# Optimization experiments

Measured on AMD Instinct MI355X. Metric: run time of the kernel, lower is better.

The kernel has to match this reference:

```python
import jax, jax.numpy as jnp
import numpy as np


def _cdist_p2(x, y):
    # x: [N, t1, h], y: [N, t2, h] -> [N, t1, t2] Euclidean distances
    x2 = jnp.sum(x * x, axis=-1)  # [N, t1]
    y2 = jnp.sum(y * y, axis=-1)  # [N, t2]
    xy = jnp.einsum('nik,njk->nij', x, y)  # [N, t1, t2]
    d2 = x2[:, :, None] + y2[None if False else slice(None), None, :] - 2.0 * xy
    d2 = jnp.maximum(d2, 0.0)
    return jnp.sqrt(d2)


def _solve_relaxed_wmd(scores, axis):
    # argmin + one-hot scatter + (mask*scores).mean() == sum of per-slice minima / scores.size
    idx = jnp.argmin(scores, axis=axis, keepdims=True)
    mins = jnp.take_along_axis(scores, idx, axis=axis)
    return jnp.sum(mins) / scores.size


def setup_inputs() -> dict:
    key = jax.random.key(0)
    kx, ky = jax.random.split(key)
    L, B, t1, t2, h = 4, 16, 1024, 1024, 128
    x = jax.random.normal(kx, (L, B, t1, h), dtype=jnp.float32)
    y = jax.random.normal(ky, (L, B, t2, h), dtype=jnp.float32)
    return {"x": x, "y": y}


def reference(x, y):
    L, B, t1, h = x.shape
    t2 = y.shape[2]
    xf = x.reshape(L * B, t1, h).astype(jnp.float32)
    yf = y.reshape(L * B, t2, h).astype(jnp.float32)
    scores = _cdist_p2(xf, yf)  # [L*B, t1, t2]
    forward_scores = _solve_relaxed_wmd(scores, axis=1)
    backward_scores = _solve_relaxed_wmd(scores, axis=2)
    return jnp.maximum(forward_scores, backward_scores)
```

## Files before the change

### kernel.cpp

```cpp
#include <hip/hip_runtime.h>

#define NB 64
#define T 1024
#define HD 128

#define EINF 0xFF800000u

typedef __attribute__((ext_vector_type(8))) short bf16x8;
typedef __attribute__((ext_vector_type(4))) float f32x4;

static __device__ __forceinline__ short f2bf(float f) {
    unsigned u = __float_as_uint(f);
    u += 0x7FFFu + ((u >> 16) & 1u);
    return (short)(u >> 16);
}
static __device__ __forceinline__ unsigned fenc(float f) {
    unsigned b = __float_as_uint(f);
    return b ^ (unsigned)(((int)b >> 31) | (int)0x80000000);
}
static __device__ __forceinline__ float fdec(unsigned u) {
    unsigned m = (~(unsigned)((int)u >> 31)) | 0x80000000u;
    return __uint_as_float(u ^ m);
}

__global__ void wmd_prep(const float* __restrict__ y, short* __restrict__ ybf,
                         float* __restrict__ y2,
                         unsigned* __restrict__ g_colmin, unsigned* __restrict__ g_rowmin,
                         float* __restrict__ sums, unsigned* __restrict__ batch_cnt,
                         unsigned* __restrict__ g_cnt) {
    int gi = blockIdx.x * 256 + threadIdx.x;
    float4 vy = reinterpret_cast<const float4*>(y)[gi];
    short4 sy;
    sy.x = f2bf(vy.x); sy.y = f2bf(vy.y); sy.z = f2bf(vy.z); sy.w = f2bf(vy.w);
    reinterpret_cast<short4*>(ybf)[gi] = sy;
    float py = vy.x * vy.x + vy.y * vy.y + vy.z * vy.z + vy.w * vy.w;
    py += __shfl_xor(py, 1);  py += __shfl_xor(py, 2);  py += __shfl_xor(py, 4);
    py += __shfl_xor(py, 8);  py += __shfl_xor(py, 16);
    if ((threadIdx.x & 31) == 0) y2[gi >> 5] = py;
    if (gi < NB * T) { g_colmin[gi] = EINF; g_rowmin[gi] = EINF; }
    if (gi < 2) sums[gi] = 0.f;
    if (gi >= 4 && gi < 4 + NB) batch_cnt[gi - 4] = 0u;
    if (gi == 4 + NB) g_cnt[0] = 0u;
}

__global__ __launch_bounds__(256, 4)
void wmd_main(const float* __restrict__ x, const short* __restrict__ ybf,
              const float* __restrict__ y2g,
              unsigned* __restrict__ g_colmin, unsigned* __restrict__ g_rowmin,
              float* __restrict__ sums, unsigned* __restrict__ batch_cnt,
              unsigned* __restrict__ g_cnt, float* __restrict__ out) {
    __shared__ short b_sm[4][32 * 128];
    __shared__ float y2_sm[512];
    __shared__ float x2_sm[128];
    __shared__ unsigned col_min_sm[512];
    __shared__ unsigned last_sm;
    __shared__ float red_sm[8];

    const int tid  = threadIdx.x;
    const int lin  = blockIdx.y * 16 + blockIdx.x;
    const int m    = (lin >> 3) & 7;
    const int grp  = ((lin >> 6) << 3) | (lin & 7);
    const int n    = grp >> 1;
    const int i0   = m * 128;
    const int j0   = (grp & 1) * 512;
    const int lane = tid & 63;
    const int wave = tid >> 6;
    const int l16  = lane & 15, quad = lane >> 4;
    const float FINF = __uint_as_float(0x7F800000u);

    #pragma unroll
    for (int e = tid; e < 512; e += 256) col_min_sm[e] = EINF;

#define ISSUE_GLLS(pbuf, jtile)                                                   \
    {                                                                             \
        const short* ybase = ybf + (((size_t)(n * T + j0 + (jtile) * 32)) << 7);  \
        _Pragma("unroll")                                                         \
        for (int it = 0; it < 2; ++it) {                                          \
            int g   = wave * 2 + it;                                              \
            int s   = g * 64 + lane;                                              \
            int row = s >> 4;                                                     \
            int c   = (s & 15) ^ (row & 7);                                       \
            const short* gp = ybase + row * 128 + c * 8;                          \
            __builtin_amdgcn_global_load_lds(                                     \
                (const __attribute__((address_space(1))) void*)gp,                \
                (__attribute__((address_space(3))) void*)&b_sm[pbuf][g * 512],    \
                16, 0, 0);                                                        \
        }                                                                         \
    }

    ISSUE_GLLS(0, 0);
    ISSUE_GLLS(1, 1);
    ISSUE_GLLS(2, 2);

    bf16x8 af[2][4];
    #pragma unroll
    for (int mi = 0; mi < 2; ++mi) {
        float part = 0.f;
        #pragma unroll
        for (int kk = 0; kk < 4; ++kk) {
            const float4* gp = reinterpret_cast<const float4*>(
                x + (((size_t)(n * T + i0 + wave * 32 + mi * 16 + l16)) << 7) + kk * 32 + quad * 8);
            float4 a = gp[0], b = gp[1];
            bf16x8 f;
            f[0] = f2bf(a.x); f[1] = f2bf(a.y); f[2] = f2bf(a.z); f[3] = f2bf(a.w);
            f[4] = f2bf(b.x); f[5] = f2bf(b.y); f[6] = f2bf(b.z); f[7] = f2bf(b.w);
            af[mi][kk] = f;
            part += a.x * a.x + a.y * a.y + a.z * a.z + a.w * a.w;
            part += b.x * b.x + b.y * b.y + b.z * b.z + b.w * b.w;
        }
        part += __shfl_xor(part, 16);
        part += __shfl_xor(part, 32);
        if (quad == 0) x2_sm[wave * 32 + mi * 16 + l16] = part;
    }
    #pragma unroll
    for (int e = tid; e < 512; e += 256) y2_sm[e] = y2g[n * T + j0 + e];

    float rmin[8];
    #pragma unroll
    for (int q = 0; q < 8; ++q) rmin[q] = FINF;

    __syncthreads();

    float x2v[8];
    #pragma unroll
    for (int mi = 0; mi < 2; ++mi)
        #pragma unroll
        for (int r = 0; r < 4; ++r)
            x2v[mi * 4 + r] = x2_sm[wave * 32 + mi * 16 + quad * 4 + r];

    for (int jt = 0; jt < 16; ++jt) {
        const int p = jt & 3;
        if (jt < 13) ISSUE_GLLS((jt + 3) & 3, jt + 3);

        float y2v[2];
        #pragma unroll
        for (int ni = 0; ni < 2; ++ni)
            y2v[ni] = y2_sm[jt * 32 + ni * 16 + l16];

        f32x4 acc[2][2];
        #pragma unroll
        for (int mi = 0; mi < 2; ++mi)
            #pragma unroll
            for (int ni = 0; ni < 2; ++ni) {
                f32x4 z = {0.f, 0.f, 0.f, 0.f};
                acc[mi][ni] = z;
            }

        #pragma unroll
        for (int kk = 0; kk < 4; ++kk) {
            bf16x8 bv[2];
            #pragma unroll
            for (int ni = 0; ni < 2; ++ni) {
                int row = ni * 16 + l16;
                int c   = (kk * 4 + quad) ^ (row & 7);
                bv[ni] = *reinterpret_cast<const bf16x8*>(&b_sm[p][(row * 16 + c) * 8]);
            }
            #pragma unroll
            for (int mi = 0; mi < 2; ++mi)
                #pragma unroll
                for (int ni = 0; ni < 2; ++ni)
                    acc[mi][ni] = __builtin_amdgcn_mfma_f32_16x16x32_bf16(
                        af[mi][kk], bv[ni], acc[mi][ni], 0, 0, 0);
        }

        float vcol[2] = {FINF, FINF};
        #pragma unroll
        for (int mi = 0; mi < 2; ++mi)
            #pragma unroll
            for (int r = 0; r < 4; ++r) {
                float x2r = x2v[mi * 4 + r];
                #pragma unroll
                for (int ni = 0; ni < 2; ++ni) {
                    float xy = acc[mi][ni][r];
                    rmin[mi * 4 + r] = fminf(rmin[mi * 4 + r], fmaf(-2.f, xy, y2v[ni]));
                    vcol[ni]         = fminf(vcol[ni],         fmaf(-2.f, xy, x2r));
                }
            }
        #pragma unroll
        for (int ni = 0; ni < 2; ++ni) {
            float v = vcol[ni];
            v = fminf(v, __shfl_xor(v, 16));
            v = fminf(v, __shfl_xor(v, 32));
            if (lane < 16)
                atomicMin(&col_min_sm[jt * 32 + ni * 16 + lane], fenc(v));
        }

        if (jt < 15) {
            if (jt <= 12)      asm volatile("s_waitcnt vmcnt(4)" ::: "memory");
            else if (jt == 13) asm volatile("s_waitcnt vmcnt(2)" ::: "memory");
            else               asm volatile("s_waitcnt vmcnt(0)" ::: "memory");
            __builtin_amdgcn_s_barrier();
            asm volatile("" ::: "memory");
        }
    }

    __syncthreads();
    #pragma unroll
    for (int e = tid; e < 512; e += 256) {
        float v = fdec(col_min_sm[e]) + y2_sm[e];
        atomicMin(&g_colmin[n * T + j0 + e], fenc(v));
    }
    #pragma unroll
    for (int mi = 0; mi < 2; ++mi)
        #pragma unroll
        for (int r = 0; r < 4; ++r) {
            float v = rmin[mi * 4 + r] + x2v[mi * 4 + r];
            v = fminf(v, __shfl_xor(v, 1));
            v = fminf(v, __shfl_xor(v, 2));
            v = fminf(v, __shfl_xor(v, 4));
            v = fminf(v, __shfl_xor(v, 8));
            if (l16 == 0)
                atomicMin(&g_rowmin[n * T + i0 + wave * 32 + mi * 16 + quad * 4 + r], fenc(v));
        }

    __builtin_amdgcn_s_waitcnt(0);
    __syncthreads();
    if (tid == 0)
        last_sm = __hip_atomic_fetch_add(&batch_cnt[n], 1u, __ATOMIC_RELAXED,
                                         __HIP_MEMORY_SCOPE_AGENT);
    __syncthreads();
    if (last_sm != 15u) return;

    float sc = 0.f, sr = 0.f;
    for (int e = tid; e < T; e += 256) {
        unsigned cu = __hip_atomic_load(&g_colmin[n * T + e], __ATOMIC_RELAXED,
                                        __HIP_MEMORY_SCOPE_AGENT);
        unsigned ru = __hip_atomic_load(&g_rowmin[n * T + e], __ATOMIC_RELAXED,
                                        __HIP_MEMORY_SCOPE_AGENT);
        sc += sqrtf(fmaxf(fdec(cu), 0.f));
        sr += sqrtf(fmaxf(fdec(ru), 0.f));
    }
    #pragma unroll
    for (int o = 1; o < 64; o <<= 1) {
        sc += __shfl_xor(sc, o);
        sr += __shfl_xor(sr, o);
    }
    if (lane == 0) { red_sm[wave] = sc; red_sm[4 + wave] = sr; }
    __syncthreads();
    if (tid == 0) {
        atomicAdd(&sums[0], red_sm[0] + red_sm[1] + red_sm[2] + red_sm[3]);
        atomicAdd(&sums[1], red_sm[4] + red_sm[5] + red_sm[6] + red_sm[7]);
        __builtin_amdgcn_s_waitcnt(0);
        unsigned old = __hip_atomic_fetch_add(g_cnt, 1u, __ATOMIC_RELAXED,
                                              __HIP_MEMORY_SCOPE_AGENT);
        if (old == NB - 1) {
            float a = __hip_atomic_load(&sums[0], __ATOMIC_RELAXED, __HIP_MEMORY_SCOPE_AGENT);
            float b = __hip_atomic_load(&sums[1], __ATOMIC_RELAXED, __HIP_MEMORY_SCOPE_AGENT);
            out[0] = fmaxf(a, b) * (1.0f / 67108864.0f);
        }
    }
}

extern "C" void kernel_launch(void* const* d_in, const int* in_sizes, int n_in,
                              void* d_out, int out_size, void* d_ws, size_t ws_size,
                              hipStream_t stream) {
    const float* x = (const float*)d_in[0];
    const float* y = (const float*)d_in[1];
    float* out = (float*)d_out;

    char* ws = (char*)d_ws;
    unsigned* g_colmin  = (unsigned*)(ws);
    unsigned* g_rowmin  = (unsigned*)(ws + 256 * 1024);
    float*    y2g       = (float*)(ws + 512 * 1024);
    float*    sums      = (float*)(ws + 768 * 1024);
    unsigned* batch_cnt = (unsigned*)(ws + 768 * 1024 + 256);
    unsigned* g_cnt     = (unsigned*)(ws + 768 * 1024 + 2048);
    short*    ybf       = (short*)(ws + 1024 * 1024);

    wmd_prep<<<(NB * T * HD / 4) / 256, 256, 0, stream>>>(
        y, ybf, y2g, g_colmin, g_rowmin, sums, batch_cnt, g_cnt);
    wmd_main<<<dim3(16, NB), 256, 0, stream>>>(
        x, ybf, y2g, g_colmin, g_rowmin, sums, batch_cnt, g_cnt, out);
}
```

Before: 128.4 us.

## Split column range into quarters, double-buffer B, raise occupancy to 8 blocks

Each block now covers 128 rows by 256 columns instead of 512, so the grid doubles to 2048 one-dimensional blocks, with a new block-to-batch mapping that interleaves batches. The four-stage LDS prefetch ring becomes a two-buffer ping-pong with a plain __syncthreads per tile, which shrinks shared memory and allows launch bounds of 8 blocks per CU. The aim is to fill the GPU with more concurrent blocks and hide latency through occupancy rather than deep prefetch. The cost is that each block reloads and reconverts its x rows twice as often, and prefetch depth drops to a single tile.

```diff
diff --git a/kernel.cpp b/kernel.cpp
--- a/kernel.cpp
+++ b/kernel.cpp
@@ -43,33 +43,33 @@
     if (gi == 4 + NB) g_cnt[0] = 0u;
 }
 
-__global__ __launch_bounds__(256, 4)
+__global__ __launch_bounds__(256, 8)
 void wmd_main(const float* __restrict__ x, const short* __restrict__ ybf,
               const float* __restrict__ y2g,
               unsigned* __restrict__ g_colmin, unsigned* __restrict__ g_rowmin,
               float* __restrict__ sums, unsigned* __restrict__ batch_cnt,
               unsigned* __restrict__ g_cnt, float* __restrict__ out) {
-    __shared__ short b_sm[4][32 * 128];
-    __shared__ float y2_sm[512];
+    __shared__ short b_sm[2][32 * 128];
+    __shared__ float y2_sm[256];
     __shared__ float x2_sm[128];
-    __shared__ unsigned col_min_sm[512];
+    __shared__ unsigned col_min_sm[256];
     __shared__ unsigned last_sm;
     __shared__ float red_sm[8];
 
     const int tid  = threadIdx.x;
-    const int lin  = blockIdx.y * 16 + blockIdx.x;
-    const int m    = (lin >> 3) & 7;
-    const int grp  = ((lin >> 6) << 3) | (lin & 7);
-    const int n    = grp >> 1;
+    const int bid  = blockIdx.x;
+    const int n    = ((bid & 7) << 3) | ((bid >> 3) & 7);
+    const int tle  = bid >> 6;
+    const int m    = tle >> 2;
+    const int jq   = tle & 3;
     const int i0   = m * 128;
-    const int j0   = (grp & 1) * 512;
+    const int j0   = jq * 256;
     const int lane = tid & 63;
     const int wave = tid >> 6;
     const int l16  = lane & 15, quad = lane >> 4;
     const float FINF = __uint_as_float(0x7F800000u);
 
-    #pragma unroll
-    for (int e = tid; e < 512; e += 256) col_min_sm[e] = EINF;
+    if (tid < 256) col_min_sm[tid] = EINF;
 
 #define ISSUE_GLLS(pbuf, jtile)                                                   \
     {                                                                             \
@@ -89,8 +89,6 @@
     }
 
     ISSUE_GLLS(0, 0);
-    ISSUE_GLLS(1, 1);
-    ISSUE_GLLS(2, 2);
 
     bf16x8 af[2][4];
     #pragma unroll
@@ -112,8 +110,7 @@
         part += __shfl_xor(part, 32);
         if (quad == 0) x2_sm[wave * 32 + mi * 16 + l16] = part;
     }
-    #pragma unroll
-    for (int e = tid; e < 512; e += 256) y2_sm[e] = y2g[n * T + j0 + e];
+    if (tid < 256) y2_sm[tid] = y2g[n * T + j0 + tid];
 
     float rmin[8];
     #pragma unroll
@@ -128,9 +125,9 @@
         for (int r = 0; r < 4; ++r)
             x2v[mi * 4 + r] = x2_sm[wave * 32 + mi * 16 + quad * 4 + r];
 
-    for (int jt = 0; jt < 16; ++jt) {
-        const int p = jt & 3;
-        if (jt < 13) ISSUE_GLLS((jt + 3) & 3, jt + 3);
+    for (int jt = 0; jt < 8; ++jt) {
+        const int p = jt & 1;
+        if (jt < 7) ISSUE_GLLS(p ^ 1, jt + 1);
 
         float y2v[2];
         #pragma unroll
@@ -184,21 +181,12 @@
             if (lane < 16)
                 atomicMin(&col_min_sm[jt * 32 + ni * 16 + lane], fenc(v));
         }
-
-        if (jt < 15) {
-            if (jt <= 12)      asm volatile("s_waitcnt vmcnt(4)" ::: "memory");
-            else if (jt == 13) asm volatile("s_waitcnt vmcnt(2)" ::: "memory");
-            else               asm volatile("s_waitcnt vmcnt(0)" ::: "memory");
-            __builtin_amdgcn_s_barrier();
-            asm volatile("" ::: "memory");
-        }
-    }
-
-    __syncthreads();
-    #pragma unroll
-    for (int e = tid; e < 512; e += 256) {
-        float v = fdec(col_min_sm[e]) + y2_sm[e];
-        atomicMin(&g_colmin[n * T + j0 + e], fenc(v));
+        __syncthreads();
+    }
+
+    if (tid < 256) {
+        float v = fdec(col_min_sm[tid]) + y2_sm[tid];
+        atomicMin(&g_colmin[n * T + j0 + tid], fenc(v));
     }
     #pragma unroll
     for (int mi = 0; mi < 2; ++mi)
@@ -219,7 +207,7 @@
         last_sm = __hip_atomic_fetch_add(&batch_cnt[n], 1u, __ATOMIC_RELAXED,
                                          __HIP_MEMORY_SCOPE_AGENT);
     __syncthreads();
-    if (last_sm != 15u) return;
+    if (last_sm != 31u) return;
 
     float sc = 0.f, sr = 0.f;
     for (int e = tid; e < T; e += 256) {
@@ -269,6 +257,6 @@
 
     wmd_prep<<<(NB * T * HD / 4) / 256, 256, 0, stream>>>(
         y, ybf, y2g, g_colmin, g_rowmin, sums, batch_cnt, g_cnt);
-    wmd_main<<<dim3(16, NB), 256, 0, stream>>>(
+    wmd_main<<<dim3(2048), 256, 0, stream>>>(
         x, ybf, y2g, g_colmin, g_rowmin, sums, batch_cnt, g_cnt, out);
 }
```

Result: slower. 436.9 us (+240.2%).
